# Performance work log

Hardware: AMD Instinct MI355X
Metric: run time of the kernel (lower is better)

The kernel has to match this reference:

```python
import jax, jax.numpy as jnp
import numpy as np

D_MODEL, HEADS, D_FF = 768, 12, 3072
D_K = D_MODEL // HEADS
EPS = 1e-6


def _norm(x, alpha, bias):
    # NormalizationLayer: scalar alpha/bias, torch.std is unbiased (ddof=1)
    mean = jnp.mean(x, axis=-1, keepdims=True)
    std = jnp.std(x, axis=-1, ddof=1, keepdims=True)
    return alpha * (x - mean) / (std + EPS) + bias


def setup_inputs() -> dict:
    key = jax.random.key(0)
    ks = jax.random.split(key, 16)
    B, S = 2, 4096
    x = jax.random.normal(ks[0], (B, S, D_MODEL), dtype=jnp.float32)
    mask = jax.random.randint(ks[1], (B, 1, 1, S), 0, 2, dtype=jnp.int32)
    w = lambda k, o, i: (jax.random.normal(k, (o, i), dtype=jnp.float32) * 0.02)
    return {
        "x": x, "mask": mask,
        "wq": w(ks[2], D_MODEL, D_MODEL), "bq": jnp.zeros((D_MODEL,), jnp.float32),
        "wk": w(ks[3], D_MODEL, D_MODEL), "bk": jnp.zeros((D_MODEL,), jnp.float32),
        "wv": w(ks[4], D_MODEL, D_MODEL), "bv": jnp.zeros((D_MODEL,), jnp.float32),
        "wo": w(ks[5], D_MODEL, D_MODEL), "bo": jnp.zeros((D_MODEL,), jnp.float32),
        "w1": w(ks[6], D_FF, D_MODEL), "b1": jnp.zeros((D_FF,), jnp.float32),
        "w2": w(ks[7], D_MODEL, D_FF), "b2": jnp.zeros((D_MODEL,), jnp.float32),
        "alpha1": jnp.ones((1,), jnp.float32), "beta1": jnp.ones((1,), jnp.float32),
        "alpha2": jnp.ones((1,), jnp.float32), "beta2": jnp.ones((1,), jnp.float32),
    }


def reference(x, mask, wq, bq, wk, bk, wv, bv, wo, bo, w1, b1, w2, b2,
              alpha1, beta1, alpha2, beta2):
    B, S, _ = x.shape

    # --- residual connection 0: pre-norm + self-attention ---
    h = _norm(x, alpha1, beta1)
    q = (h @ wq.T + bq).reshape(B, S, HEADS, D_K).transpose(0, 2, 1, 3)  # [B,H,S,dk]
    k = (h @ wk.T + bk).reshape(B, S, HEADS, D_K).transpose(0, 2, 1, 3)
    v = (h @ wv.T + bv).reshape(B, S, HEADS, D_K).transpose(0, 2, 1, 3)
    scores = jnp.einsum('bhqd,bhkd->bhqk', q, k) / jnp.sqrt(jnp.float32(D_K))
    scores = jnp.where(mask == 0, jnp.float32(-1e9), scores)
    attn = jax.nn.softmax(scores, axis=-1)
    ctx = jnp.einsum('bhqk,bhkd->bhqd', attn, v)
    ctx = ctx.transpose(0, 2, 1, 3).reshape(B, S, D_MODEL)
    x = x + (ctx @ wo.T + bo)

    # --- residual connection 1: pre-norm + FFN ---
    h = _norm(x, alpha2, beta2)
    ff = jax.nn.relu(h @ w1.T + b1) @ w2.T + b2
    return x + ff
```

## Files before the change

### kernel.cpp

```cpp
#include <hip/hip_runtime.h>
#include <hip/hip_bf16.h>
#include <math.h>


typedef __hip_bfloat16 bf16;
typedef short short8 __attribute__((ext_vector_type(8)));
typedef short short4v __attribute__((ext_vector_type(4)));
typedef float f32x4 __attribute__((ext_vector_type(4)));

#define MFMA(A, B, C) __builtin_amdgcn_mfma_f32_16x16x32_bf16(A, B, C, 0, 0, 0)

#if __has_builtin(__builtin_amdgcn_exp2f)
#define EXP2(x) __builtin_amdgcn_exp2f(x)
#else
#define EXP2(x) exp2f(x)
#endif

#define PSWAP32(a, b) asm("v_permlane32_swap_b32 %0, %1" : "+v"(a), "+v"(b))
#define PSWAP16(a, b) asm("v_permlane16_swap_b32 %0, %1" : "+v"(a), "+v"(b))

__device__ __forceinline__ unsigned cvt_pk(float lo, float hi) {
  unsigned r;
  asm("v_cvt_pk_bf16_f32 %0, %1, %2" : "=v"(r) : "v"(lo), "v"(hi));
  return r;
}

__device__ __forceinline__ void gl_lds16(const void* g, void* l) {
  __builtin_amdgcn_global_load_lds(
      (__attribute__((address_space(1))) void*)g,
      (__attribute__((address_space(3))) void*)l, 16, 0, 0);
}

__device__ __forceinline__ short f2b(float f) {
  bf16 h = __float2bfloat16(f);
  return *reinterpret_cast<short*>(&h);
}

__global__ __launch_bounds__(256)
void prep_all(const float* __restrict__ wq, const float* __restrict__ wk,
              const float* __restrict__ wv, const float* __restrict__ wo,
              const float* __restrict__ w1, const float* __restrict__ w2,
              const float* __restrict__ bq, const float* __restrict__ bk,
              const float* __restrict__ bv, const int* __restrict__ mask,
              bf16* __restrict__ wqkvb, bf16* __restrict__ wob,
              bf16* __restrict__ w1b, bf16* __restrict__ w2b,
              float* __restrict__ bqkv,
              int* __restrict__ pos_g, int* __restrict__ nch_g,
              bf16* __restrict__ kc, bf16* __restrict__ vtc)
{
  const int t = threadIdx.x;
  if (blockIdx.x < 2) {
    const int b = blockIdx.x;
    const int* mb = mask + b * 4096;
    __shared__ int lsum[256];
    int loc = 0;
    int mv[16];
#pragma unroll
    for (int j = 0; j < 16; j++) { mv[j] = mb[t * 16 + j] ? 1 : 0; loc += mv[j]; }
    lsum[t] = loc;
    __syncthreads();
    for (int off = 1; off < 256; off <<= 1) {
      int v = (t >= off) ? lsum[t - off] : 0;
      __syncthreads();
      lsum[t] += v;
      __syncthreads();
    }
    const int nvalid = lsum[255];
    int base = lsum[t] - loc;
#pragma unroll
    for (int j = 0; j < 16; j++) {
      pos_g[b * 4096 + t * 16 + j] = mv[j] ? base : -1;
      if (mv[j]) base++;
    }
    const int npad = (nvalid + 63) & ~63;
    if (t == 0) { nch_g[b * 2] = npad >> 6; nch_g[b * 2 + 1] = npad - nvalid; }
    const int npv = npad - nvalid;
    if (npv > 0) {
      const int krows = 12 * npv;
      const short8 z = {};
      for (int task = t; task < krows * 8; task += 256) {
        const int rr = task >> 3, cc = task & 7;
        const int hh = rr / npv, r = nvalid + rr % npv;
        *(short8*)&kc[(((long)(b * 12 + hh) * 4096) + r) * 64 + cc * 8] = z;
      }
      const int vrows = 12 * 64;
      for (int task = t; task < vrows * npv; task += 256) {
        const int row = task / npv, j = nvalid + task % npv;
        const int hh = row >> 6, d = row & 63;
        vtc[((long)((b * 12 + hh) * 64 + d)) * 4096 + j] = __float2bfloat16(0.f);
      }
    }
    return;
  }
  const int i = (blockIdx.x - 2) * 256 + t;
  const int W = 147456;
  const int F = 589824;
  const float* src; bf16* dst; int off;
  if (i < W)          { src = wq; dst = wqkvb;           off = i; }
  else if (i < 2*W)   { src = wk; dst = wqkvb + 589824;  off = i - W; }
  else if (i < 3*W)   { src = wv; dst = wqkvb + 1179648; off = i - 2*W; }
  else if (i < 4*W)   { src = wo; dst = wob;             off = i - 3*W; }
  else if (i < 4*W+F) { src = w1; dst = w1b;             off = i - 4*W; }
  else                { src = w2; dst = w2b;             off = i - 4*W - F; }
  float4 v = ((const float4*)src)[off];
  short4v o;
  o.x = f2b(v.x); o.y = f2b(v.y); o.z = f2b(v.z); o.w = f2b(v.w);
  ((short4v*)dst)[off] = o;
  if (i < 2304)
    bqkv[i] = (i < 768) ? bq[i] : (i < 1536 ? bk[i - 768] : bv[i - 1536]);
}

template<typename INT>
__global__ __launch_bounds__(256)
void ln_kernel(const INT* __restrict__ x, bf16* __restrict__ out,
               const float* __restrict__ alpha, const float* __restrict__ beta)
{
  const int row = blockIdx.x;
  const long base = (long)row * 768;
  const int t = threadIdx.x;
  float v[3]; float s = 0.f, ss = 0.f;
#pragma unroll
  for (int i = 0; i < 3; i++) {
    v[i] = (float)x[base + t + i * 256];
    s += v[i]; ss += v[i] * v[i];
  }
#pragma unroll
  for (int off = 32; off > 0; off >>= 1) {
    s  += __shfl_down(s, off);
    ss += __shfl_down(ss, off);
  }
  __shared__ float red[8];
  __shared__ float stats[2];
  const int w = t >> 6;
  if ((t & 63) == 0) { red[w] = s; red[4 + w] = ss; }
  __syncthreads();
  if (t == 0) {
    float S  = red[0] + red[1] + red[2] + red[3];
    float SS = red[4] + red[5] + red[6] + red[7];
    float mean = S * (1.f / 768.f);
    float var = fmaxf((SS - 768.f * mean * mean) * (1.f / 767.f), 0.f);
    stats[0] = mean;
    stats[1] = 1.f / (sqrtf(var) + 1e-6f);
  }
  __syncthreads();
  const float mean = stats[0], rinv = stats[1];
  const float a = alpha[0], b = beta[0];
#pragma unroll
  for (int i = 0; i < 3; i++)
    out[base + t + i * 256] = __float2bfloat16(a * (v[i] - mean) * rinv + b);
}

template<int MODE, int TM, typename RT, typename OUTT>
__global__ __launch_bounds__(256)
void gemm_bt(const bf16* __restrict__ A, const bf16* __restrict__ W,
             const float* __restrict__ bias, const RT* __restrict__ R,
             OUTT* __restrict__ Cout, int M, int N, int K)
{
  constexpr int MI = TM / 32;
  __shared__ __align__(16) bf16 sA[2][TM * 32];
  __shared__ __align__(16) bf16 sB[2][128 * 32];
  const int t = threadIdx.x;
  const int w = t >> 6, lane = t & 63;
  const int lr = lane & 15, quad = lane >> 4;
  const int tm = blockIdx.x * TM, tn = blockIdx.y * 128;
  const int wm = (w >> 1) * (MI * 16), wn = (w & 1) * 64;

  const int srow = w * 16 + (lane >> 2);
  const int scol = (lane & 3) * 8;
  const int soff = srow * 32 + scol;
  const bf16* Ap = A + (long)(tm + srow) * K + scol;
  const bf16* Wp = W + (long)(tn + srow) * K + scol;
  const long half = (long)64 * K;

  auto stage = [&](int kb, int bi) {
    gl_lds16(Ap + kb, &sA[bi][soff]);
    if (TM == 128) gl_lds16(Ap + kb + half, &sA[bi][soff + 64 * 32]);
    gl_lds16(Wp + kb, &sB[bi][soff]);
    gl_lds16(Wp + kb + half, &sB[bi][soff + 64 * 32]);
  };

  f32x4 acc[MI][4] = {};

  stage(0, 0);
  int bi = 0;
  for (int kb = 0; kb < K; kb += 32, bi ^= 1) {
    __syncthreads();
    if (kb + 32 < K) stage(kb + 32, bi ^ 1);
    const bf16* sAb = sA[bi];
    const bf16* sBb = sB[bi];
    short8 af[MI], bfr[4];
#pragma unroll
    for (int i = 0; i < MI; i++)
      af[i] = *(const short8*)&sAb[(wm + i * 16 + lr) * 32 + quad * 8];
#pragma unroll
    for (int j = 0; j < 4; j++)
      bfr[j] = *(const short8*)&sBb[(wn + j * 16 + lr) * 32 + quad * 8];
#pragma unroll
    for (int i = 0; i < MI; i++)
#pragma unroll
      for (int j = 0; j < 4; j++)
        acc[i][j] = MFMA(af[i], bfr[j], acc[i][j]);
  }

#pragma unroll
  for (int i = 0; i < MI; i++) {
#pragma unroll
    for (int j = 0; j < 4; j++) {
      const int col = tn + wn + j * 16 + lr;
      const float bv = bias[col];
#pragma unroll
      for (int r = 0; r < 4; r++) {
        const int m = tm + wm + i * 16 + quad * 4 + r;
        float vv = acc[i][j][r] + bv;
        if (MODE == 1) vv = fmaxf(vv, 0.f);
        if (MODE == 4) vv += (float)R[(long)m * N + col];
        Cout[(long)m * N + col] = (OUTT)vv;
      }
    }
  }
}

__global__ __launch_bounds__(256)
void gemm_qkv(const bf16* __restrict__ A, const bf16* __restrict__ W,
              const float* __restrict__ bias, const int* __restrict__ pos_g,
              bf16* __restrict__ Qo, bf16* __restrict__ Kc, bf16* __restrict__ Vtc)
{
  const int K = 768;
  __shared__ __align__(16) bf16 sA[2][128 * 32];
  __shared__ __align__(16) bf16 sB[2][128 * 32];
  const int t = threadIdx.x;
  const int w = t >> 6, lane = t & 63;
  const int lr = lane & 15, quad = lane >> 4;
  const int tm = blockIdx.x * 128, tn = blockIdx.y * 128;
  const int wm = (w >> 1) * 64, wn = (w & 1) * 64;

  const int srow = w * 16 + (lane >> 2);
  const int scol = (lane & 3) * 8;
  const int soff = srow * 32 + scol;
  const bf16* Ap = A + (long)(tm + srow) * K + scol;
  const bf16* Wp = W + (long)(tn + srow) * K + scol;
  const long half = (long)64 * K;

  auto stage = [&](int kb, int bi) {
    gl_lds16(Ap + kb, &sA[bi][soff]);
    gl_lds16(Ap + kb + half, &sA[bi][soff + 64 * 32]);
    gl_lds16(Wp + kb, &sB[bi][soff]);
    gl_lds16(Wp + kb + half, &sB[bi][soff + 64 * 32]);
  };

  f32x4 acc[4][4] = {};

  stage(0, 0);
  int bi = 0;
  for (int kb = 0; kb < K; kb += 32, bi ^= 1) {
    __syncthreads();
    if (kb + 32 < K) stage(kb + 32, bi ^ 1);
    const bf16* sAb = sA[bi];
    const bf16* sBb = sB[bi];
    short8 af[4], bfr[4];
#pragma unroll
    for (int i = 0; i < 4; i++)
      af[i] = *(const short8*)&sAb[(wm + i * 16 + lr) * 32 + quad * 8];
#pragma unroll
    for (int j = 0; j < 4; j++)
      bfr[j] = *(const short8*)&sBb[(wn + j * 16 + lr) * 32 + quad * 8];
#pragma unroll
    for (int i = 0; i < 4; i++)
#pragma unroll
      for (int j = 0; j < 4; j++)
        acc[i][j] = MFMA(af[i], bfr[j], acc[i][j]);
  }

  const int region = (tn >= 1536) ? 2 : (tn >= 768 ? 1 : 0);
#pragma unroll
  for (int i = 0; i < 4; i++) {
#pragma unroll
    for (int j = 0; j < 4; j++) {
      const int col = tn + wn + j * 16 + lr;
      const int c768 = col - region * 768;
      const int hh = c768 >> 6, d = c768 & 63;
      const float bv = bias[col];
#pragma unroll
      for (int r = 0; r < 4; r++) {
        const int m = tm + wm + i * 16 + quad * 4 + r;
        const int bb = m >> 12, sdx = m & 4095;
        float vv = acc[i][j][r] + bv;
        if (region == 0) {
          vv *= 0.18033688011112042f;
          Qo[((long)(bb * 12 + hh) * 4096 + sdx) * 64 + d] = __float2bfloat16(vv);
        } else {
          const int p_ = pos_g[bb * 4096 + sdx];
          if (p_ >= 0) {
            if (region == 1)
              Kc[((long)(bb * 12 + hh) * 4096 + p_) * 64 + d] = __float2bfloat16(vv);
            else
              Vtc[((long)(bb * 12 + hh) * 64 + d) * 4096 + p_] = __float2bfloat16(vv);
          }
        }
      }
    }
  }
}

__global__ __launch_bounds__(256)
void attn_kernel(const bf16* __restrict__ Q, const bf16* __restrict__ Kg,
                 const bf16* __restrict__ Vt,
                 const int* __restrict__ nch_g, bf16* __restrict__ ctx)
{
  __shared__ __align__(16) bf16 sK[2][64 * 64];
  __shared__ __align__(16) bf16 sV[2][64 * 64];

  const int t = threadIdx.x, w = t >> 6, lane = t & 63;
  const int lr = lane & 15, quad = lane >> 4;
  const int bh = blockIdx.y, b = bh / 12, hh = bh % 12;
  const int qb = blockIdx.x * 128 + w * 32;
  const long bh_s = (long)bh * 4096;
  const int nch = nch_g[b * 2];
  const int npv = nch_g[b * 2 + 1];

  short8 qf[2][2];
#pragma unroll
  for (int qt = 0; qt < 2; qt++) {
    const bf16* qp = Q + (bh_s + qb + qt * 16 + lr) * 64 + quad * 8;
    qf[qt][0] = *(const short8*)qp;
    qf[qt][1] = *(const short8*)(qp + 32);
  }

  short8 ones;
#pragma unroll
  for (int i = 0; i < 8; i++) ones[i] = (short)0x3F80;

  const int rA = w * 16 + (lane >> 3), rB = rA + 8;
  const int c8 = lane & 7;
  const bf16* kA = Kg + (bh_s + rA) * 64 + ((c8 ^ (rA & 7)) << 3);
  const bf16* kB = Kg + (bh_s + rB) * 64 + ((c8 ^ (rB & 7)) << 3);
  const bf16* vA = Vt + ((long)bh * 64 + rA) * 4096 + ((c8 ^ (rA & 7)) << 3);
  const bf16* vB = Vt + ((long)bh * 64 + rB) * 4096 + ((c8 ^ (rB & 7)) << 3);
  const int ldsA = (w * 16) * 64 + lane * 8;
  const int ldsB = ldsA + 8 * 64;

  const int cA = (quad * 8) ^ ((lr & 7) << 3);

  f32x4 lacc[2] = {};
  f32x4 Ot[4][2] = {};

  auto stage = [&](int kc, int buf) {
    gl_lds16(kA + (long)kc * 64, &sK[buf][ldsA]);
    gl_lds16(kB + (long)kc * 64, &sK[buf][ldsB]);
    gl_lds16(vA + kc, &sV[buf][ldsA]);
    gl_lds16(vB + kc, &sV[buf][ldsB]);
  };

  auto compute = [&](int buf) {
    const bf16* Kb = sK[buf];
    const bf16* Vb = sV[buf];
    f32x4 st[4][2] = {};
    __builtin_amdgcn_s_setprio(1);
#pragma unroll
    for (int kt = 0; kt < 4; kt++) {
      const int rowb = (kt * 16 + lr) * 64;
      short8 kfa = *(const short8*)&Kb[rowb + cA];
      short8 kfb = *(const short8*)&Kb[rowb + (cA ^ 32)];
      st[kt][0] = MFMA(kfa, qf[0][0], st[kt][0]);
      st[kt][0] = MFMA(kfb, qf[0][1], st[kt][0]);
      st[kt][1] = MFMA(kfa, qf[1][0], st[kt][1]);
      st[kt][1] = MFMA(kfb, qf[1][1], st[kt][1]);
    }
    __builtin_amdgcn_s_setprio(0);

    short8 pf[2][2];
#pragma unroll
    for (int qt = 0; qt < 2; qt++) {
      float p[4][4];
#pragma unroll
      for (int kt = 0; kt < 4; kt++)
#pragma unroll
        for (int r = 0; r < 4; r++)
          p[kt][r] = EXP2(st[kt][qt][r]);
      unsigned u00 = cvt_pk(p[0][0], p[0][1]), u01 = cvt_pk(p[0][2], p[0][3]);
      unsigned u10 = cvt_pk(p[1][0], p[1][1]), u11 = cvt_pk(p[1][2], p[1][3]);
      unsigned u20 = cvt_pk(p[2][0], p[2][1]), u21 = cvt_pk(p[2][2], p[2][3]);
      unsigned u30 = cvt_pk(p[3][0], p[3][1]), u31 = cvt_pk(p[3][2], p[3][3]);
      PSWAP32(u00, u10); PSWAP32(u01, u11);
      PSWAP32(u20, u30); PSWAP32(u21, u31);
      PSWAP16(u00, u10); PSWAP16(u01, u11);
      PSWAP16(u20, u30); PSWAP16(u21, u31);
      union { unsigned u[4]; short8 s8; } fa, fb;
      fa.u[0] = u00; fa.u[1] = u01; fa.u[2] = u10; fa.u[3] = u11;
      fb.u[0] = u20; fb.u[1] = u21; fb.u[2] = u30; fb.u[3] = u31;
      pf[qt][0] = fa.s8;
      pf[qt][1] = fb.s8;
    }

    __builtin_amdgcn_s_setprio(1);
#pragma unroll
    for (int dt = 0; dt < 4; dt++) {
      const int rowb = (dt * 16 + lr) * 64;
      short8 vfa = *(const short8*)&Vb[rowb + cA];
      short8 vfb = *(const short8*)&Vb[rowb + (cA ^ 32)];
      Ot[dt][0] = MFMA(vfa, pf[0][0], Ot[dt][0]);
      Ot[dt][0] = MFMA(vfb, pf[0][1], Ot[dt][0]);
      Ot[dt][1] = MFMA(vfa, pf[1][0], Ot[dt][1]);
      Ot[dt][1] = MFMA(vfb, pf[1][1], Ot[dt][1]);
    }
    lacc[0] = MFMA(ones, pf[0][0], lacc[0]);
    lacc[0] = MFMA(ones, pf[0][1], lacc[0]);
    lacc[1] = MFMA(ones, pf[1][0], lacc[1]);
    lacc[1] = MFMA(ones, pf[1][1], lacc[1]);
    __builtin_amdgcn_s_setprio(0);
  };

  stage(0, 0);
  for (int ci = 0; ci < nch; ci++) {
    __syncthreads();
    if (ci + 1 < nch) stage((ci + 1) * 64, (ci + 1) & 1);
    compute(ci & 1);
  }

#pragma unroll
  for (int qt = 0; qt < 2; qt++) {
    const float l = lacc[qt][0] - (float)npv;
    const float il = (l > 0.f) ? 1.f / l : 0.f;
    const int q = qb + qt * 16 + lr;
    bf16* cp = ctx + ((long)(b * 4096 + q)) * 768 + hh * 64 + quad * 4;
#pragma unroll
    for (int dt = 0; dt < 4; dt++) {
      short4v ov;
      ov.x = f2b(Ot[dt][qt][0] * il);
      ov.y = f2b(Ot[dt][qt][1] * il);
      ov.z = f2b(Ot[dt][qt][2] * il);
      ov.w = f2b(Ot[dt][qt][3] * il);
      *(short4v*)(cp + dt * 16) = ov;
    }
  }
}

extern "C" void kernel_launch(void* const* d_in, const int* in_sizes, int n_in,
                              void* d_out, int out_size, void* d_ws, size_t ws_size,
                              hipStream_t stream)
{
  (void)in_sizes; (void)n_in; (void)out_size; (void)ws_size;
  const float* x    = (const float*)d_in[0];
  const int*   mask = (const int*)  d_in[1];
  const float* wq = (const float*)d_in[2];  const float* bq = (const float*)d_in[3];
  const float* wk = (const float*)d_in[4];  const float* bk = (const float*)d_in[5];
  const float* wv = (const float*)d_in[6];  const float* bv = (const float*)d_in[7];
  const float* wo = (const float*)d_in[8];  const float* bo = (const float*)d_in[9];
  const float* w1 = (const float*)d_in[10]; const float* b1 = (const float*)d_in[11];
  const float* w2 = (const float*)d_in[12]; const float* b2 = (const float*)d_in[13];
  const float* alpha1 = (const float*)d_in[14]; const float* beta1 = (const float*)d_in[15];
  const float* alpha2 = (const float*)d_in[16]; const float* beta2 = (const float*)d_in[17];
  float* out = (float*)d_out;

  const long WSZ = (long)768 * 768 * 2;
  const long W1SZ = (long)3072 * 768 * 2;
  const long SZB = (long)8192 * 768 * 2;
  char* ws = (char*)d_ws;
  bf16* wqkvb = (bf16*)(ws);
  bf16* wob = (bf16*)(ws + 3 * WSZ);
  bf16* w1b = (bf16*)(ws + 4 * WSZ);
  bf16* w2b = (bf16*)(ws + 4 * WSZ + W1SZ);
  char* aux = ws + 4 * WSZ + 2 * W1SZ;
  float* bqkv   = (float*)(aux);
  int*   pos_g  = (int*)(aux + 16384);
  int*   nch_g  = (int*)(aux + 81920);
  const long BASE = 16l << 20;
  bf16* h   = (bf16*)(ws + BASE);
  bf16* qws = (bf16*)(ws + BASE + 1 * SZB);
  bf16* kcw = (bf16*)(ws + BASE + 2 * SZB);
  bf16* vtc = (bf16*)(ws + BASE + 3 * SZB);
  bf16* ctx = (bf16*)(ws + BASE + 4 * SZB);
  bf16* x1  = (bf16*)(ws + BASE + 5 * SZB);
  bf16* ff  = qws;

  dim3 blk(256);

  hipLaunchKernelGGL(prep_all, dim3(6914), blk, 0, stream,
                     wq, wk, wv, wo, w1, w2, bq, bk, bv, mask,
                     wqkvb, wob, w1b, w2b, bqkv, pos_g, nch_g, kcw, vtc);

  hipLaunchKernelGGL((ln_kernel<float>), dim3(8192), blk, 0, stream, x, h, alpha1, beta1);
  hipLaunchKernelGGL(gemm_qkv, dim3(64, 18), blk, 0, stream, h, wqkvb, bqkv, pos_g, qws, kcw, vtc);
  hipLaunchKernelGGL(attn_kernel, dim3(32, 24), blk, 0, stream, qws, kcw, vtc, nch_g, ctx);
  hipLaunchKernelGGL((gemm_bt<4, 64, float, bf16>), dim3(128, 6), blk, 0, stream, ctx, wob, bo, x, x1, 8192, 768, 768);
  hipLaunchKernelGGL((ln_kernel<bf16>), dim3(8192), blk, 0, stream, x1, h, alpha2, beta2);
  hipLaunchKernelGGL((gemm_bt<1, 128, float, bf16>), dim3(64, 24), blk, 0, stream, h, w1b, b1, (const float*)nullptr, ff, 8192, 3072, 768);
  hipLaunchKernelGGL((gemm_bt<4, 64, bf16, float>), dim3(128, 6), blk, 0, stream, ff, w2b, b2, x1, out, 8192, 768, 3072);
}
```

Baseline: 398.0 us.

## Use 2-wave attention blocks with 64 query rows per wave

The attention kernel now runs 128 threads per block, and each wave processes 64 query rows instead of 32, so the block still covers 128 queries. Every K/V fragment read from LDS is reused across four query tiles instead of two, which halves LDS read traffic per MFMA. Each thread stages four K/V rows per chunk instead of two, and the QK^T computation is reordered per query tile. The cost is more accumulator registers (16 Ot tiles plus hoisted K fragments), which may lower occupancy, and fewer waves per block to hide latency.

```diff
diff --git a/kernel.cpp b/kernel.cpp
--- a/kernel.cpp
+++ b/kernel.cpp
@@ -302,7 +302,7 @@
   }
 }
 
-__global__ __launch_bounds__(256)
+__global__ __launch_bounds__(128)
 void attn_kernel(const bf16* __restrict__ Q, const bf16* __restrict__ Kg,
                  const bf16* __restrict__ Vt,
                  const int* __restrict__ nch_g, bf16* __restrict__ ctx)
@@ -313,14 +313,14 @@
   const int t = threadIdx.x, w = t >> 6, lane = t & 63;
   const int lr = lane & 15, quad = lane >> 4;
   const int bh = blockIdx.y, b = bh / 12, hh = bh % 12;
-  const int qb = blockIdx.x * 128 + w * 32;
+  const int qb = blockIdx.x * 128 + w * 64;
   const long bh_s = (long)bh * 4096;
   const int nch = nch_g[b * 2];
   const int npv = nch_g[b * 2 + 1];
 
-  short8 qf[2][2];
-#pragma unroll
-  for (int qt = 0; qt < 2; qt++) {
+  short8 qf[4][2];
+#pragma unroll
+  for (int qt = 0; qt < 4; qt++) {
     const bf16* qp = Q + (bh_s + qb + qt * 16 + lr) * 64 + quad * 8;
     qf[qt][0] = *(const short8*)qp;
     qf[qt][1] = *(const short8*)(qp + 32);
@@ -330,53 +330,58 @@
 #pragma unroll
   for (int i = 0; i < 8; i++) ones[i] = (short)0x3F80;
 
-  const int rA = w * 16 + (lane >> 3), rB = rA + 8;
+  const int rOff = lane >> 3;
   const int c8 = lane & 7;
-  const bf16* kA = Kg + (bh_s + rA) * 64 + ((c8 ^ (rA & 7)) << 3);
-  const bf16* kB = Kg + (bh_s + rB) * 64 + ((c8 ^ (rB & 7)) << 3);
-  const bf16* vA = Vt + ((long)bh * 64 + rA) * 4096 + ((c8 ^ (rA & 7)) << 3);
-  const bf16* vB = Vt + ((long)bh * 64 + rB) * 4096 + ((c8 ^ (rB & 7)) << 3);
-  const int ldsA = (w * 16) * 64 + lane * 8;
-  const int ldsB = ldsA + 8 * 64;
+  const int scw = (c8 ^ rOff) << 3;
+  const bf16* kP[4]; const bf16* vP[4]; int ldsO[4];
+#pragma unroll
+  for (int j = 0; j < 4; j++) {
+    const int r = w * 32 + j * 8 + rOff;
+    kP[j] = Kg + (bh_s + r) * 64 + scw;
+    vP[j] = Vt + ((long)bh * 64 + r) * 4096 + scw;
+    ldsO[j] = (w * 32 + j * 8) * 64 + lane * 8;
+  }
 
   const int cA = (quad * 8) ^ ((lr & 7) << 3);
 
-  f32x4 lacc[2] = {};
-  f32x4 Ot[4][2] = {};
+  f32x4 lacc[4] = {};
+  f32x4 Ot[4][4] = {};
 
   auto stage = [&](int kc, int buf) {
-    gl_lds16(kA + (long)kc * 64, &sK[buf][ldsA]);
-    gl_lds16(kB + (long)kc * 64, &sK[buf][ldsB]);
-    gl_lds16(vA + kc, &sV[buf][ldsA]);
-    gl_lds16(vB + kc, &sV[buf][ldsB]);
+#pragma unroll
+    for (int j = 0; j < 4; j++) {
+      gl_lds16(kP[j] + (long)kc * 64, &sK[buf][ldsO[j]]);
+      gl_lds16(vP[j] + kc, &sV[buf][ldsO[j]]);
+    }
   };
 
   auto compute = [&](int buf) {
     const bf16* Kb = sK[buf];
     const bf16* Vb = sV[buf];
-    f32x4 st[4][2] = {};
-    __builtin_amdgcn_s_setprio(1);
+    short8 kf0[4], kf1[4];
 #pragma unroll
     for (int kt = 0; kt < 4; kt++) {
       const int rowb = (kt * 16 + lr) * 64;
-      short8 kfa = *(const short8*)&Kb[rowb + cA];
-      short8 kfb = *(const short8*)&Kb[rowb + (cA ^ 32)];
-      st[kt][0] = MFMA(kfa, qf[0][0], st[kt][0]);
-      st[kt][0] = MFMA(kfb, qf[0][1], st[kt][0]);
-      st[kt][1] = MFMA(kfa, qf[1][0], st[kt][1]);
-      st[kt][1] = MFMA(kfb, qf[1][1], st[kt][1]);
-    }
-    __builtin_amdgcn_s_setprio(0);
-
-    short8 pf[2][2];
-#pragma unroll
-    for (int qt = 0; qt < 2; qt++) {
+      kf0[kt] = *(const short8*)&Kb[rowb + cA];
+      kf1[kt] = *(const short8*)&Kb[rowb + (cA ^ 32)];
+    }
+    short8 pf[4][2];
+#pragma unroll
+    for (int qt = 0; qt < 4; qt++) {
+      f32x4 st[4] = {};
+      __builtin_amdgcn_s_setprio(1);
+#pragma unroll
+      for (int kt = 0; kt < 4; kt++) {
+        st[kt] = MFMA(kf0[kt], qf[qt][0], st[kt]);
+        st[kt] = MFMA(kf1[kt], qf[qt][1], st[kt]);
+      }
+      __builtin_amdgcn_s_setprio(0);
       float p[4][4];
 #pragma unroll
       for (int kt = 0; kt < 4; kt++)
 #pragma unroll
         for (int r = 0; r < 4; r++)
-          p[kt][r] = EXP2(st[kt][qt][r]);
+          p[kt][r] = EXP2(st[kt][r]);
       unsigned u00 = cvt_pk(p[0][0], p[0][1]), u01 = cvt_pk(p[0][2], p[0][3]);
       unsigned u10 = cvt_pk(p[1][0], p[1][1]), u11 = cvt_pk(p[1][2], p[1][3]);
       unsigned u20 = cvt_pk(p[2][0], p[2][1]), u21 = cvt_pk(p[2][2], p[2][3]);
@@ -398,15 +403,17 @@
       const int rowb = (dt * 16 + lr) * 64;
       short8 vfa = *(const short8*)&Vb[rowb + cA];
       short8 vfb = *(const short8*)&Vb[rowb + (cA ^ 32)];
-      Ot[dt][0] = MFMA(vfa, pf[0][0], Ot[dt][0]);
-      Ot[dt][0] = MFMA(vfb, pf[0][1], Ot[dt][0]);
-      Ot[dt][1] = MFMA(vfa, pf[1][0], Ot[dt][1]);
-      Ot[dt][1] = MFMA(vfb, pf[1][1], Ot[dt][1]);
-    }
-    lacc[0] = MFMA(ones, pf[0][0], lacc[0]);
-    lacc[0] = MFMA(ones, pf[0][1], lacc[0]);
-    lacc[1] = MFMA(ones, pf[1][0], lacc[1]);
-    lacc[1] = MFMA(ones, pf[1][1], lacc[1]);
+#pragma unroll
+      for (int qt = 0; qt < 4; qt++) {
+        Ot[dt][qt] = MFMA(vfa, pf[qt][0], Ot[dt][qt]);
+        Ot[dt][qt] = MFMA(vfb, pf[qt][1], Ot[dt][qt]);
+      }
+    }
+#pragma unroll
+    for (int qt = 0; qt < 4; qt++) {
+      lacc[qt] = MFMA(ones, pf[qt][0], lacc[qt]);
+      lacc[qt] = MFMA(ones, pf[qt][1], lacc[qt]);
+    }
     __builtin_amdgcn_s_setprio(0);
   };
 
@@ -418,7 +425,7 @@
   }
 
 #pragma unroll
-  for (int qt = 0; qt < 2; qt++) {
+  for (int qt = 0; qt < 4; qt++) {
     const float l = lacc[qt][0] - (float)npv;
     const float il = (l > 0.f) ? 1.f / l : 0.f;
     const int q = qb + qt * 16 + lr;
@@ -481,7 +488,7 @@
 
   hipLaunchKernelGGL((ln_kernel<float>), dim3(8192), blk, 0, stream, x, h, alpha1, beta1);
   hipLaunchKernelGGL(gemm_qkv, dim3(64, 18), blk, 0, stream, h, wqkvb, bqkv, pos_g, qws, kcw, vtc);
-  hipLaunchKernelGGL(attn_kernel, dim3(32, 24), blk, 0, stream, qws, kcw, vtc, nch_g, ctx);
+  hipLaunchKernelGGL(attn_kernel, dim3(32, 24), dim3(128), 0, stream, qws, kcw, vtc, nch_g, ctx);
   hipLaunchKernelGGL((gemm_bt<4, 64, float, bf16>), dim3(128, 6), blk, 0, stream, ctx, wob, bo, x, x1, 8192, 768, 768);
   hipLaunchKernelGGL((ln_kernel<bf16>), dim3(8192), blk, 0, stream, x1, h, alpha2, beta2);
   hipLaunchKernelGGL((gemm_bt<1, 128, float, bf16>), dim3(64, 24), blk, 0, stream, h, w1b, b1, (const float*)nullptr, ff, 8192, 3072, 768);
```

After: 415.8 us. +4.5%, slower.

## Split attention over two key halves and merge partial results

Applied to the files above, without the earlier changes.

The attention launch gets a grid z-dimension of 2, and each block handles half of the compacted key chunks. Each half writes unnormalized bf16 output plus its row sums, and a new combine kernel adds the halves and divides by the total normalizer. The aim is to double the number of blocks (768 to 1536) for better occupancy across the CUs. The cost is an extra kernel launch, extra memory traffic for the partial buffers, and bf16 rounding of unnormalized partial sums. It also relies on there being no running max, which holds because the softmax here is computed without max subtraction.

```diff
diff --git a/kernel.cpp b/kernel.cpp
--- a/kernel.cpp
+++ b/kernel.cpp
@@ -34,6 +34,11 @@
 __device__ __forceinline__ short f2b(float f) {
   bf16 h = __float2bfloat16(f);
   return *reinterpret_cast<short*>(&h);
+}
+
+__device__ __forceinline__ float b2f(short s) {
+  bf16 h = *reinterpret_cast<bf16*>(&s);
+  return __bfloat162float(h);
 }
 
 __global__ __launch_bounds__(256)
@@ -305,7 +310,9 @@
 __global__ __launch_bounds__(256)
 void attn_kernel(const bf16* __restrict__ Q, const bf16* __restrict__ Kg,
                  const bf16* __restrict__ Vt,
-                 const int* __restrict__ nch_g, bf16* __restrict__ ctx)
+                 const int* __restrict__ nch_g,
+                 bf16* __restrict__ ctx, bf16* __restrict__ part,
+                 float* __restrict__ lbuf)
 {
   __shared__ __align__(16) bf16 sK[2][64 * 64];
   __shared__ __align__(16) bf16 sV[2][64 * 64];
@@ -313,10 +320,13 @@
   const int t = threadIdx.x, w = t >> 6, lane = t & 63;
   const int lr = lane & 15, quad = lane >> 4;
   const int bh = blockIdx.y, b = bh / 12, hh = bh % 12;
+  const int kh = blockIdx.z;
   const int qb = blockIdx.x * 128 + w * 32;
   const long bh_s = (long)bh * 4096;
   const int nch = nch_g[b * 2];
-  const int npv = nch_g[b * 2 + 1];
+  const int c0 = (nch + 1) >> 1;
+  const int cbeg = kh ? c0 : 0;
+  const int cend = kh ? nch : c0;
 
   short8 qf[2][2];
 #pragma unroll
@@ -410,29 +420,54 @@
     __builtin_amdgcn_s_setprio(0);
   };
 
-  stage(0, 0);
-  for (int ci = 0; ci < nch; ci++) {
-    __syncthreads();
-    if (ci + 1 < nch) stage((ci + 1) * 64, (ci + 1) & 1);
-    compute(ci & 1);
-  }
-
+  if (cbeg < cend) {
+    stage(cbeg * 64, 0);
+    for (int ci = cbeg; ci < cend; ci++) {
+      __syncthreads();
+      if (ci + 1 < cend) stage((ci + 1) * 64, (ci + 1 - cbeg) & 1);
+      compute((ci - cbeg) & 1);
+    }
+  }
+
+  bf16* outp = kh ? part : ctx;
 #pragma unroll
   for (int qt = 0; qt < 2; qt++) {
-    const float l = lacc[qt][0] - (float)npv;
-    const float il = (l > 0.f) ? 1.f / l : 0.f;
     const int q = qb + qt * 16 + lr;
-    bf16* cp = ctx + ((long)(b * 4096 + q)) * 768 + hh * 64 + quad * 4;
+    if (quad == 0)
+      lbuf[((long)(kh * 2 + b) * 12 + hh) * 4096 + q] = lacc[qt][0];
+    bf16* cp = outp + ((long)(b * 4096 + q)) * 768 + hh * 64 + quad * 4;
 #pragma unroll
     for (int dt = 0; dt < 4; dt++) {
       short4v ov;
-      ov.x = f2b(Ot[dt][qt][0] * il);
-      ov.y = f2b(Ot[dt][qt][1] * il);
-      ov.z = f2b(Ot[dt][qt][2] * il);
-      ov.w = f2b(Ot[dt][qt][3] * il);
+      ov.x = f2b(Ot[dt][qt][0]);
+      ov.y = f2b(Ot[dt][qt][1]);
+      ov.z = f2b(Ot[dt][qt][2]);
+      ov.w = f2b(Ot[dt][qt][3]);
       *(short4v*)(cp + dt * 16) = ov;
     }
   }
+}
+
+__global__ __launch_bounds__(256)
+void combine_kernel(bf16* __restrict__ ctx, const bf16* __restrict__ part,
+                    const float* __restrict__ lbuf, const int* __restrict__ nch_g)
+{
+  const int e = blockIdx.x * 256 + threadIdx.x;
+  const int row = e / 96;
+  const int c8 = e - row * 96;
+  const int hh = c8 >> 3;
+  const int b = row >> 12, q = row & 4095;
+  const float l0 = lbuf[((long)b * 12 + hh) * 4096 + q];
+  const float l1 = lbuf[((long)(2 + b) * 12 + hh) * 4096 + q];
+  const float l = l0 + l1 - (float)nch_g[b * 2 + 1];
+  const float il = (l > 0.f) ? 1.f / l : 0.f;
+  short8 a = ((const short8*)ctx)[e];
+  short8 p = ((const short8*)part)[e];
+  short8 o;
+#pragma unroll
+  for (int j = 0; j < 8; j++)
+    o[j] = f2b((b2f(a[j]) + b2f(p[j])) * il);
+  ((short8*)ctx)[e] = o;
 }
 
 extern "C" void kernel_launch(void* const* d_in, const int* in_sizes, int n_in,
@@ -464,6 +499,7 @@
   float* bqkv   = (float*)(aux);
   int*   pos_g  = (int*)(aux + 16384);
   int*   nch_g  = (int*)(aux + 81920);
+  float* lbuf   = (float*)(aux + 98304);
   const long BASE = 16l << 20;
   bf16* h   = (bf16*)(ws + BASE);
   bf16* qws = (bf16*)(ws + BASE + 1 * SZB);
@@ -472,6 +508,7 @@
   bf16* ctx = (bf16*)(ws + BASE + 4 * SZB);
   bf16* x1  = (bf16*)(ws + BASE + 5 * SZB);
   bf16* ff  = qws;
+  bf16* part = h;
 
   dim3 blk(256);
 
@@ -481,7 +518,8 @@
 
   hipLaunchKernelGGL((ln_kernel<float>), dim3(8192), blk, 0, stream, x, h, alpha1, beta1);
   hipLaunchKernelGGL(gemm_qkv, dim3(64, 18), blk, 0, stream, h, wqkvb, bqkv, pos_g, qws, kcw, vtc);
-  hipLaunchKernelGGL(attn_kernel, dim3(32, 24), blk, 0, stream, qws, kcw, vtc, nch_g, ctx);
+  hipLaunchKernelGGL(attn_kernel, dim3(32, 24, 2), blk, 0, stream, qws, kcw, vtc, nch_g, ctx, part, lbuf);
+  hipLaunchKernelGGL(combine_kernel, dim3(3072), blk, 0, stream, ctx, part, lbuf, nch_g);
   hipLaunchKernelGGL((gemm_bt<4, 64, float, bf16>), dim3(128, 6), blk, 0, stream, ctx, wob, bo, x, x1, 8192, 768, 768);
   hipLaunchKernelGGL((ln_kernel<bf16>), dim3(8192), blk, 0, stream, x1, h, alpha2, beta2);
   hipLaunchKernelGGL((gemm_bt<1, 128, float, bf16>), dim3(64, 24), blk, 0, stream, h, w1b, b1, (const float*)nullptr, ff, 8192, 3072, 768);
```

New measurement: 409.3 us. +2.8%, slower.
